# Optimization experiments

Hardware: AMD Instinct MI355X
Metric: run time of the kernel (lower is better)

Reference implementation:

```python
import jax, jax.numpy as jnp
import numpy as np

B, S, N, F = 4, 8, 1024, 6
H, L, K, D = 64, 3, 16, 3  # hidden, layers, neighbors, num_dims
EPS = 1e-6


def setup_inputs() -> dict:
    key = jax.random.key(0)
    ks = iter(jax.random.split(key, 64))

    def w(shape, fan_in):
        return jax.random.normal(next(ks), shape, jnp.float32) / np.sqrt(fan_in)

    inp = {
        'points': jax.random.normal(next(ks), (B, S, N, F), jnp.float32),
        'w_in': w((F, H), F), 'b_in': jnp.zeros((H,), jnp.float32),
        # stacked per-layer params for the 3 PointTransformerLayers
        'Wq': w((L, H, H), H), 'bq': jnp.zeros((L, H), jnp.float32),
        'Wk': w((L, H, H), H), 'bk': jnp.zeros((L, H), jnp.float32),
        'Wv': w((L, H, H), H), 'bv': jnp.zeros((L, H), jnp.float32),
        'Wpe': w((L, D, H), D), 'bpe': jnp.zeros((L, H), jnp.float32),
        'Wpd': w((L, D, H), D), 'bpd': jnp.zeros((L, H), jnp.float32),
        'Wa': w((L, H, 1), H), 'ba': jnp.zeros((L, 1), jnp.float32),
        'Wo': w((L, H, H), H), 'bo': jnp.zeros((L, H), jnp.float32),
        'ln_s': jnp.ones((L, H), jnp.float32), 'ln_b': jnp.zeros((L, H), jnp.float32),
        # EncoderTransformerLayer params
        'Wek': w((H, H), H), 'bek': jnp.zeros((H,), jnp.float32),
        'Weq': w((H, H), H), 'beq': jnp.zeros((H,), jnp.float32),
        'Wev': w((H, H), H), 'bev': jnp.zeros((H,), jnp.float32),
        'We1': w((H, H), H), 'be1': jnp.zeros((H,), jnp.float32),
        'We2': w((H, H), H), 'be2': jnp.zeros((H,), jnp.float32),
        'ln2_s': jnp.ones((H,), jnp.float32), 'ln2_b': jnp.zeros((H,), jnp.float32),
    }
    return inp


def _layernorm(x, scale, bias):
    mu = jnp.mean(x, axis=-1, keepdims=True)
    var = jnp.var(x, axis=-1, keepdims=True)
    return (x - mu) * jax.lax.rsqrt(var + EPS) * scale + bias


def _point_layer(x, pos, Wq, bq, Wk, bk, Wv, bv, Wpe, bpe, Wpd, bpd, Wa, ba, Wo, bo):
    # x: [B,S,N,H], pos: [B,S,N,3]
    q = x @ Wq + bq
    k = x @ Wk + bk
    v = x @ Wv + bv
    pos_enc = pos @ Wpe + bpe  # [B,S,N,H]
    # pairwise squared distances: diff[i,j] = pos[i] - pos[j]
    pos_diff = pos[..., :, None, :] - pos[..., None, :, :]  # [B,S,N,N,3]
    dist = jnp.sum(pos_diff ** 2, axis=-1)                  # [B,S,N,N]
    _, nidx = jax.lax.top_k(-dist, K)                       # [B,S,N,K]

    def gather(a):  # a: [B,S,N,C] -> [B,S,N,K,C]
        return jnp.take_along_axis(a[:, :, None], nidx[..., None], axis=3)

    k_n = gather(k)
    v_n = gather(v)
    p_n = gather(pos_enc)
    qp = (q + pos_enc)[..., None, :]                        # [B,S,N,1,H]
    pd_enc = (gather(pos) - pos[..., None, :]) @ Wpd + bpd  # [B,S,N,K,H]
    scale = jnp.sqrt(jnp.float32(H))
    attn = qp * (k_n + p_n + pd_enc) / scale                # [B,S,N,K,H]
    attn = (attn @ Wa + ba).squeeze(-1)                     # [B,S,N,K]
    attn = jax.nn.softmax(attn, axis=-1)
    out = jnp.sum(attn[..., None] * v_n, axis=-2)           # [B,S,N,H]
    out = jax.nn.gelu(out @ Wo + bo)
    return x + out


def _encoder_layer(x, Wek, bek, Weq, beq, Wev, bev, We1, be1, We2, be2):
    k = x @ Wek + bek
    q = x @ Weq + beq
    v = x @ Wev + bev
    aw = jnp.einsum('bth,bsh->bts', q, k)
    aw = jax.nn.softmax(aw / jnp.sqrt(jnp.float32(H)), axis=-1)
    out = jnp.einsum('bts,bsh->bth', aw, v)
    out = jax.nn.gelu(out @ We1 + be1) @ We2 + be2
    return x + out


def reference(points, w_in, b_in, Wq, bq, Wk, bk, Wv, bv, Wpe, bpe, Wpd, bpd,
              Wa, ba, Wo, bo, ln_s, ln_b, Wek, bek, Weq, beq, Wev, bev,
              We1, be1, We2, be2, ln2_s, ln2_b):
    pos = points[..., :D]
    x = points @ w_in + b_in
    for i in range(L):
        x = _point_layer(x, pos, Wq[i], bq[i], Wk[i], bk[i], Wv[i], bv[i],
                         Wpe[i], bpe[i], Wpd[i], bpd[i], Wa[i], ba[i], Wo[i], bo[i])
        x = _layernorm(x, ln_s[i], ln_b[i])
    x = jnp.max(x, axis=-2)  # pool over points -> [B,S,H]
    x = _encoder_layer(x, Wek, bek, Weq, beq, Wev, bev, We1, be1, We2, be2)
    x = _layernorm(x, ln2_s, ln2_b)
    x = jnp.max(x, axis=-2)  # pool over seq -> [B,H]
    return x
```

## Files before the change

kernel.cpp:

```cpp
#include <hip/hip_runtime.h>
#include <cfloat>
#include <cmath>
#include <cstdint>

#define NPT   1024
#define NCL   32
#define PTOT  32768
#define HH    64
#define KNN_K 16
#define KNN_BLKS (NCL * 256)

#define RFL(x) __builtin_amdgcn_readfirstlane(x)

__device__ __forceinline__ float wave_sum64(float t) {
#pragma unroll
  for (int o = 32; o > 0; o >>= 1) t += __shfl_xor(t, o, 64);
  return t;
}

template <int NV>
__device__ __forceinline__ float mreduce(const float (&P)[NV], int lane) {
  float buf[NV];
#pragma unroll
  for (int i = 0; i < NV; ++i) buf[i] = P[i];
#pragma unroll
  for (int s = 0; (1 << s) < NV; ++s) {
    bool hi = (lane & (1 << s)) != 0;
#pragma unroll
    for (int m = 0; m < (NV >> (s + 1)); ++m) {
      float a = buf[2 * m], b = buf[2 * m + 1];
      float keep = hi ? b : a;
      float send = hi ? a : b;
      buf[m] = keep + __shfl_xor(send, 1 << s, 64);
    }
  }
  float t = buf[0];
#pragma unroll
  for (int o = NV; o < 64; o <<= 1) t += __shfl_xor(t, o, 64);
  return t;
}

__device__ __forceinline__ float gelu_f(float z) {
  float zc = 0.7978845608028654f * (z + 0.044715f * z * z * z);
  float t = __expf(2.0f * zc);
  float th = 1.0f - 2.0f / (t + 1.0f);
  return 0.5f * z * (1.0f + th);
}

__global__ __launch_bounds__(256) void k_front(
    const float* __restrict__ pts, const float* __restrict__ w_in,
    const float* __restrict__ b_in, float* __restrict__ x,
    float* __restrict__ pos4, int* __restrict__ nidx) {
  if (blockIdx.x >= KNN_BLKS) {
    int b2 = blockIdx.x - KNN_BLKS;
    int vb = (b2 & 7) * 1024 + (b2 >> 3);
    int p = vb * 4 + (threadIdx.x >> 6);
    int h = threadIdx.x & 63;
    const float* pp = pts + p * 6;
    float acc = b_in[h];
#pragma unroll
    for (int f = 0; f < 6; ++f) acc += pp[f] * w_in[f * HH + h];
    x[p * HH + h] = acc;
    if (h < 4) pos4[p * 4 + h] = (h < 3) ? pp[h] : 0.0f;
    return;
  }

  __shared__ float4 sp[NPT];
  int cloud = blockIdx.x >> 8;
  int qbase = (blockIdx.x & 255) * 4;
  const float* cp = pts + (size_t)cloud * NPT * 6;
  for (int j = threadIdx.x; j < NPT; j += 256) {
    const float* q = cp + j * 6;
    sp[j] = make_float4(q[0], q[1], q[2], 0.0f);
  }
  __syncthreads();

  int wv = threadIdx.x >> 6;
  int lane = threadIdx.x & 63;
  int i = qbase + wv;
  float4 qp = sp[i];

  unsigned du[16];
#pragma unroll
  for (int c = 0; c < 16; ++c) {
    float4 pj = sp[c * 64 + lane];
    float dx = qp.x - pj.x, dy = qp.y - pj.y, dz = qp.z - pj.z;
    float d2 = __fadd_rn(__fadd_rn(__fmul_rn(dx, dx), __fmul_rn(dy, dy)),
                         __fmul_rn(dz, dz));
    du[c] = __float_as_uint(d2);
  }

  unsigned t = 0u;
#pragma unroll
  for (int bit = 30; bit >= 15; --bit) {
    unsigned tp = t | (1u << bit);
    int cnt = 0;
#pragma unroll
    for (int c = 0; c < 16; ++c)
      cnt += __popcll(__ballot(du[c] < tp));
    if (cnt <= 15) t = tp;
  }

  int obase = (cloud * NPT + i) * KNN_K;
  unsigned long long below = (1ull << lane) - 1ull;
  int slot = 0;
#pragma unroll
  for (int c = 0; c < 16; ++c) {
    bool lt = du[c] < t;
    unsigned long long m = __ballot(lt);
    if (lt) {
      int off = __popcll(m & below);
      nidx[obase + slot + off] = c * 64 + lane;
    }
    slot += __popcll(m);
  }

  int erem = KNN_K - slot;
  unsigned hi_end = t + (1u << 15);
  unsigned bu[16];
#pragma unroll
  for (int c = 0; c < 16; ++c)
    bu[c] = (du[c] >= t && du[c] < hi_end) ? du[c] : 0xFFFFFFFFu;
  for (int r2 = 0; r2 < erem; ++r2) {
    unsigned bd = bu[0];
    int bc = 0;
#pragma unroll
    for (int c = 1; c < 16; ++c) {
      if (bu[c] < bd) { bd = bu[c]; bc = c; }
    }
    unsigned gd = bd;
#pragma unroll
    for (int o = 32; o > 0; o >>= 1) {
      unsigned g2 = (unsigned)__shfl_xor((int)gd, o, 64);
      gd = (g2 < gd) ? g2 : gd;
    }
    int myidx = bc * 64 + lane;
    int gidx = (bd == gd) ? myidx : 0x7fffffff;
#pragma unroll
    for (int o = 32; o > 0; o >>= 1) {
      int g2 = __shfl_xor(gidx, o, 64);
      gidx = (g2 < gidx) ? g2 : gidx;
    }
    if (lane == 0) nidx[obase + slot + r2] = gidx;
    int sel = (myidx == gidx) ? bc : 99;
#pragma unroll
    for (int c = 0; c < 16; ++c) bu[c] = (c == sel) ? 0xFFFFFFFFu : bu[c];
  }
}

__global__ __launch_bounds__(256) void k_qkv_gemm(
    const float* __restrict__ x, const float* __restrict__ pos4,
    const float* __restrict__ Wq, const float* __restrict__ bq,
    const float* __restrict__ Wk, const float* __restrict__ bk,
    const float* __restrict__ Wv, const float* __restrict__ bv,
    const float* __restrict__ Wpe, const float* __restrict__ bpe,
    const float* __restrict__ Wpd, const float* __restrict__ bpd,
    float* __restrict__ qq, float* __restrict__ kkv) {
  __shared__ float w_lds[3][HH][HH];
  int lane = threadIdx.x & 63;
  int wv = threadIdx.x >> 6;
  int bid = blockIdx.x;
  int vb = (bid & 7) * 128 + (bid >> 3);
  int pb = RFL(vb * 32 + wv * 8);
  const float* xw = x + (size_t)pb * HH;
  const float4* posw = reinterpret_cast<const float4*>(pos4) + pb;

  {
    float4* dst = reinterpret_cast<float4*>(&w_lds[0][0][0]);
    const float4* s0 = reinterpret_cast<const float4*>(Wq);
    const float4* s1 = reinterpret_cast<const float4*>(Wk);
    const float4* s2 = reinterpret_cast<const float4*>(Wv);
#pragma unroll
    for (int i = 0; i < 4; ++i) {
      int idx = i * 256 + threadIdx.x;
      dst[idx] = s0[idx];
      dst[1024 + idx] = s1[idx];
      dst[2048 + idx] = s2[idx];
    }
  }
  __syncthreads();

  float wpe0 = Wpe[lane], wpe1 = Wpe[HH + lane], wpe2 = Wpe[2 * HH + lane];
  float wpd0 = Wpd[lane], wpd1 = Wpd[HH + lane], wpd2 = Wpd[2 * HH + lane];
  float we0 = wpe0 + wpd0, we1 = wpe1 + wpd1, we2 = wpe2 + wpd2;
  float bqq = bq[lane] + bpe[lane];
  float bkk = bk[lane] + bpe[lane] + bpd[lane];
  float bvv = bv[lane];

  float aq[8], ak[8], av[8];
#pragma unroll
  for (int p = 0; p < 8; ++p) { aq[p] = bqq; ak[p] = bkk; av[p] = bvv; }

#pragma unroll
  for (int c = 0; c < 8; ++c) {
    float wq8[8], wk8[8], wv8[8];
#pragma unroll
    for (int j = 0; j < 8; ++j) {
      int g = c * 8 + j;
      wq8[j] = w_lds[0][g][lane];
      wk8[j] = w_lds[1][g][lane];
      wv8[j] = w_lds[2][g][lane];
    }
#pragma unroll
    for (int p = 0; p < 8; ++p) {
#pragma unroll
      for (int j = 0; j < 8; ++j) {
        float xv = xw[p * HH + c * 8 + j];
        aq[p] = fmaf(xv, wq8[j], aq[p]);
        ak[p] = fmaf(xv, wk8[j], ak[p]);
        av[p] = fmaf(xv, wv8[j], av[p]);
      }
    }
  }

#pragma unroll
  for (int p = 0; p < 8; ++p) {
    float4 pp = posw[p];
    float qv = aq[p] + pp.x * wpe0 + pp.y * wpe1 + pp.z * wpe2;
    float kv = ak[p] + pp.x * we0 + pp.y * we1 + pp.z * we2;
    qq[(size_t)(pb + p) * HH + lane] = qv;
    reinterpret_cast<float2*>(kkv + ((size_t)(pb + p) << 7))[lane] =
        make_float2(kv, av[p]);
  }
}

__global__ __launch_bounds__(256) void k_attn_core(
    float* __restrict__ qq, const float* __restrict__ kkv,
    const int* __restrict__ nidx, const float* __restrict__ pos4,
    const float* __restrict__ Wpd, const float* __restrict__ Wa,
    const float* __restrict__ ba) {
  int lane = threadIdx.x & 63;
  int bid = blockIdx.x;
  int vb = (bid & 7) * 1024 + (bid >> 3);
  int pu = RFL(vb * 4 + (threadIdx.x >> 6));
  int cbase = pu & ~(NPT - 1);

  float4 pp = reinterpret_cast<const float4*>(pos4)[pu];
  float u = qq[(size_t)pu * HH + lane] * Wa[lane] * 0.125f;
  float pdq = pp.x * Wpd[lane] + pp.y * Wpd[HH + lane] + pp.z * Wpd[2 * HH + lane];
  float C0 = wave_sum64(u * pdq) - ba[0];

  const int4* niw = reinterpret_cast<const int4*>(nidx + (size_t)pu * KNN_K);
  int nj[KNN_K];
#pragma unroll
  for (int g = 0; g < 4; ++g) {
    int4 r = niw[g];
    nj[g * 4 + 0] = r.x; nj[g * 4 + 1] = r.y;
    nj[g * 4 + 2] = r.z; nj[g * 4 + 3] = r.w;
  }

  float vj[KNN_K], P[KNN_K];
#pragma unroll
  for (int jj = 0; jj < KNN_K; ++jj) {
    float2 kv = reinterpret_cast<const float2*>(
        kkv + ((size_t)(cbase + nj[jj]) << 7))[lane];
    vj[jj] = kv.y;
    P[jj] = u * kv.x;
  }

  float T = mreduce<16>(P, lane);
  float lg = T - C0;

  float mx = lg;
#pragma unroll
  for (int o = 1; o < 16; o <<= 1) mx = fmaxf(mx, __shfl_xor(mx, o, 64));
  float e = __expf(lg - mx);
  float s = e;
#pragma unroll
  for (int o = 1; o < 16; o <<= 1) s += __shfl_xor(s, o, 64);

  float oacc = 0.f;
  int sb = lane & 48;
#pragma unroll
  for (int jj = 0; jj < KNN_K; ++jj)
    oacc = fmaf(__shfl(e, sb | jj, 64), vj[jj], oacc);

  qq[(size_t)pu * HH + lane] = oacc / s;
}

__global__ __launch_bounds__(256) void k_wo_ln(
    const float* __restrict__ outb, const float* __restrict__ Wo,
    const float* __restrict__ bo, float* __restrict__ x,
    const float* __restrict__ ln_s, const float* __restrict__ ln_b,
    float* __restrict__ partial, int do_pool) {
  __shared__ float w_lds[HH][HH];
  __shared__ float red[4][HH];
  int lane = threadIdx.x & 63;
  int wv = threadIdx.x >> 6;
  int bid = blockIdx.x;
  int vb = (bid & 7) * 128 + (bid >> 3);
  int pb = RFL(vb * 32 + wv * 8);
  const float* ow = outb + (size_t)pb * HH;

  {
    float4* dst = reinterpret_cast<float4*>(&w_lds[0][0]);
    const float4* src = reinterpret_cast<const float4*>(Wo);
#pragma unroll
    for (int i = 0; i < 4; ++i) {
      int idx = i * 256 + threadIdx.x;
      dst[idx] = src[idx];
    }
  }
  __syncthreads();

  float acc[8];
  float b0 = bo[lane];
#pragma unroll
  for (int p = 0; p < 8; ++p) acc[p] = b0;

#pragma unroll
  for (int c = 0; c < 8; ++c) {
    float w8[8];
#pragma unroll
    for (int j = 0; j < 8; ++j) w8[j] = w_lds[c * 8 + j][lane];
#pragma unroll
    for (int p = 0; p < 8; ++p) {
#pragma unroll
      for (int j = 0; j < 8; ++j) {
        float ov = ow[p * HH + c * 8 + j];
        acc[p] = fmaf(ov, w8[j], acc[p]);
      }
    }
  }

  float sg = ln_s[lane], bg = ln_b[lane];
  float xn[8];
#pragma unroll
  for (int p = 0; p < 8; ++p)
    xn[p] = x[(size_t)(pb + p) * HH + lane] + gelu_f(acc[p]);

  float Ts = mreduce<8>(xn, lane);
  float dd[8], sq[8];
#pragma unroll
  for (int p = 0; p < 8; ++p) {
    float mu = __shfl(Ts, p, 64) * (1.0f / HH);
    dd[p] = xn[p] - mu;
    sq[p] = dd[p] * dd[p];
  }
  float Tv = mreduce<8>(sq, lane);
  float mxp = -FLT_MAX;
#pragma unroll
  for (int p = 0; p < 8; ++p) {
    float var = __shfl(Tv, p, 64) * (1.0f / HH);
    float yv = dd[p] * rsqrtf(var + 1e-6f) * sg + bg;
    x[(size_t)(pb + p) * HH + lane] = yv;
    mxp = fmaxf(mxp, yv);
  }

  if (do_pool) {
    red[wv][lane] = mxp;
    __syncthreads();
    if (wv == 0) {
      float m = fmaxf(fmaxf(red[0][lane], red[1][lane]),
                      fmaxf(red[2][lane], red[3][lane]));
      partial[(size_t)vb * HH + lane] = m;
    }
  }
}

__global__ __launch_bounds__(512) void k_enc(
    const float* __restrict__ partial,
    const float* __restrict__ Wek, const float* __restrict__ bek,
    const float* __restrict__ Weq, const float* __restrict__ beq,
    const float* __restrict__ Wev, const float* __restrict__ bev,
    const float* __restrict__ We1, const float* __restrict__ be1,
    const float* __restrict__ We2, const float* __restrict__ be2,
    const float* __restrict__ ln2_s, const float* __restrict__ ln2_b,
    float* __restrict__ out) {
  __shared__ float xs[8][HH], ks[8][HH], vs[8][HH], x2[8][HH];
  int b = blockIdx.x;
  int t = threadIdx.x >> 6;
  int h = threadIdx.x & 63;
  {
    int ci = b * 8 + t;
    const float* pp = partial + (size_t)ci * 32 * HH + h;
    float mx = pp[0];
#pragma unroll
    for (int c8 = 1; c8 < 32; ++c8) mx = fmaxf(mx, pp[c8 * HH]);
    xs[t][h] = mx;
  }
  __syncthreads();

  float kk = bek[h], qq = beq[h], vv = bev[h];
#pragma unroll 8
  for (int g = 0; g < HH; ++g) {
    float xv = xs[t][g];
    kk += xv * Wek[g * HH + h];
    qq += xv * Weq[g * HH + h];
    vv += xv * Wev[g * HH + h];
  }
  ks[t][h] = kk;
  vs[t][h] = vv;
  __syncthreads();

  float logit[8];
#pragma unroll
  for (int s = 0; s < 8; ++s) {
    float tt = qq * ks[s][h];
    logit[s] = wave_sum64(tt) * 0.125f;
  }
  float m = logit[0];
#pragma unroll
  for (int s = 1; s < 8; ++s) m = fmaxf(m, logit[s]);
  float ssum = 0.f;
#pragma unroll
  for (int s = 0; s < 8; ++s) { logit[s] = expf(logit[s] - m); ssum += logit[s]; }
  float o = 0.f;
#pragma unroll
  for (int s = 0; s < 8; ++s) o += (logit[s] / ssum) * vs[s][h];

  float h1 = be1[h];
#pragma unroll 8
  for (int g = 0; g < HH; ++g) h1 += __shfl(o, g, 64) * We1[g * HH + h];
  h1 = gelu_f(h1);
  float h2 = be2[h];
#pragma unroll 8
  for (int g = 0; g < HH; ++g) h2 += __shfl(h1, g, 64) * We2[g * HH + h];

  float xn = xs[t][h] + h2;
  float mu = wave_sum64(xn) * (1.0f / HH);
  float d = xn - mu;
  float var = wave_sum64(d * d) * (1.0f / HH);
  float yv = d * rsqrtf(var + 1e-6f) * ln2_s[h] + ln2_b[h];
  x2[t][h] = yv;
  __syncthreads();
  if (t == 0) {
    float mm = x2[0][h];
#pragma unroll
    for (int s = 1; s < 8; ++s) mm = fmaxf(mm, x2[s][h]);
    out[b * HH + h] = mm;
  }
}

extern "C" void kernel_launch(void* const* d_in, const int* in_sizes, int n_in,
                              void* d_out, int out_size, void* d_ws, size_t ws_size,
                              hipStream_t stream) {
  const float* points = (const float*)d_in[0];
  const float* w_in   = (const float*)d_in[1];
  const float* b_in   = (const float*)d_in[2];
  const float* Wq     = (const float*)d_in[3];
  const float* bq     = (const float*)d_in[4];
  const float* Wk     = (const float*)d_in[5];
  const float* bk     = (const float*)d_in[6];
  const float* Wv     = (const float*)d_in[7];
  const float* bv     = (const float*)d_in[8];
  const float* Wpe    = (const float*)d_in[9];
  const float* bpe    = (const float*)d_in[10];
  const float* Wpd    = (const float*)d_in[11];
  const float* bpd    = (const float*)d_in[12];
  const float* Wa     = (const float*)d_in[13];
  const float* ba     = (const float*)d_in[14];
  const float* Wo     = (const float*)d_in[15];
  const float* bo     = (const float*)d_in[16];
  const float* ln_s   = (const float*)d_in[17];
  const float* ln_b   = (const float*)d_in[18];
  const float* Wek    = (const float*)d_in[19];
  const float* bek    = (const float*)d_in[20];
  const float* Weq    = (const float*)d_in[21];
  const float* beq    = (const float*)d_in[22];
  const float* Wev    = (const float*)d_in[23];
  const float* bev    = (const float*)d_in[24];
  const float* We1    = (const float*)d_in[25];
  const float* be1    = (const float*)d_in[26];
  const float* We2    = (const float*)d_in[27];
  const float* be2    = (const float*)d_in[28];
  const float* ln2_s  = (const float*)d_in[29];
  const float* ln2_b  = (const float*)d_in[30];

  float* ws      = (float*)d_ws;
  float* pos4    = ws;
  float* xbuf    = pos4 + 4 * PTOT;
  float* qbuf    = xbuf + 64 * PTOT;
  float* kkv     = qbuf + 64 * PTOT;
  float* partial = kkv + 128 * PTOT;
  int*   nidx    = (int*)(partial + 2048 * HH);

  k_front<<<KNN_BLKS + PTOT / 4, 256, 0, stream>>>(points, w_in, b_in,
                                                   xbuf, pos4, nidx);

  for (int l = 0; l < 3; ++l) {
    k_qkv_gemm<<<1024, 256, 0, stream>>>(xbuf, pos4,
        Wq + l * HH * HH, bq + l * HH,
        Wk + l * HH * HH, bk + l * HH,
        Wv + l * HH * HH, bv + l * HH,
        Wpe + l * 3 * HH, bpe + l * HH,
        Wpd + l * 3 * HH, bpd + l * HH,
        qbuf, kkv);
    k_attn_core<<<PTOT / 4, 256, 0, stream>>>(qbuf, kkv, nidx, pos4,
        Wpd + l * 3 * HH, Wa + l * HH, ba + l);
    k_wo_ln<<<1024, 256, 0, stream>>>(qbuf,
        Wo + l * HH * HH, bo + l * HH, xbuf,
        ln_s + l * HH, ln_b + l * HH, partial, l == 2 ? 1 : 0);
  }

  k_enc<<<4, 512, 0, stream>>>(partial, Wek, bek, Weq, beq, Wev, bev,
                               We1, be1, We2, be2, ln2_s, ln2_b, (float*)d_out);
}
```

Before: 218.8 us.

## Fuse attention with Wo/LayerNorm and input projection with first QKV GEMM

Splits kNN into its own kernel, with each block handling 32 queries (8 per wave) so the shared-memory point load is amortised. The input projection is fused into the layer-0 QKV GEMM. The attention core is fused with the Wo projection, GELU and LayerNorm in one wave-per-point kernel, which removes the round trip of the attention output through global memory and one launch per layer. The cost is that Wo is now read directly from global/cache per wave rather than staged in LDS. Pooling partials grow 4x, so the encoder's reduction loop lengthens from 32 to 256 steps.

```diff
diff --git a/kernel.cpp b/kernel.cpp
--- a/kernel.cpp
+++ b/kernel.cpp
@@ -8,7 +8,6 @@
 #define PTOT  32768
 #define HH    64
 #define KNN_K 16
-#define KNN_BLKS (NCL * 256)
 
 #define RFL(x) __builtin_amdgcn_readfirstlane(x)
 
@@ -47,27 +46,11 @@
   return 0.5f * z * (1.0f + th);
 }
 
-__global__ __launch_bounds__(256) void k_front(
-    const float* __restrict__ pts, const float* __restrict__ w_in,
-    const float* __restrict__ b_in, float* __restrict__ x,
-    float* __restrict__ pos4, int* __restrict__ nidx) {
-  if (blockIdx.x >= KNN_BLKS) {
-    int b2 = blockIdx.x - KNN_BLKS;
-    int vb = (b2 & 7) * 1024 + (b2 >> 3);
-    int p = vb * 4 + (threadIdx.x >> 6);
-    int h = threadIdx.x & 63;
-    const float* pp = pts + p * 6;
-    float acc = b_in[h];
-#pragma unroll
-    for (int f = 0; f < 6; ++f) acc += pp[f] * w_in[f * HH + h];
-    x[p * HH + h] = acc;
-    if (h < 4) pos4[p * 4 + h] = (h < 3) ? pp[h] : 0.0f;
-    return;
-  }
-
+__global__ __launch_bounds__(256) void k_knn(const float* __restrict__ pts,
+                                             int* __restrict__ nidx) {
   __shared__ float4 sp[NPT];
-  int cloud = blockIdx.x >> 8;
-  int qbase = (blockIdx.x & 255) * 4;
+  int cloud = blockIdx.x >> 5;
+  int qbase = (blockIdx.x & 31) * 32;
   const float* cp = pts + (size_t)cloud * NPT * 6;
   for (int j = threadIdx.x; j < NPT; j += 256) {
     const float* q = cp + j * 6;
@@ -77,74 +60,167 @@
 
   int wv = threadIdx.x >> 6;
   int lane = threadIdx.x & 63;
-  int i = qbase + wv;
-  float4 qp = sp[i];
-
-  unsigned du[16];
-#pragma unroll
-  for (int c = 0; c < 16; ++c) {
-    float4 pj = sp[c * 64 + lane];
-    float dx = qp.x - pj.x, dy = qp.y - pj.y, dz = qp.z - pj.z;
-    float d2 = __fadd_rn(__fadd_rn(__fmul_rn(dx, dx), __fmul_rn(dy, dy)),
-                         __fmul_rn(dz, dz));
-    du[c] = __float_as_uint(d2);
-  }
-
-  unsigned t = 0u;
-#pragma unroll
-  for (int bit = 30; bit >= 15; --bit) {
-    unsigned tp = t | (1u << bit);
-    int cnt = 0;
+
+  for (int qi = 0; qi < 8; ++qi) {
+    int i = qbase + wv * 8 + qi;
+    float4 qp = sp[i];
+
+    unsigned du[16];
+#pragma unroll
+    for (int c = 0; c < 16; ++c) {
+      float4 pj = sp[c * 64 + lane];
+      float dx = qp.x - pj.x, dy = qp.y - pj.y, dz = qp.z - pj.z;
+      float d2 = __fadd_rn(__fadd_rn(__fmul_rn(dx, dx), __fmul_rn(dy, dy)),
+                           __fmul_rn(dz, dz));
+      du[c] = __float_as_uint(d2);
+    }
+
+    unsigned t = 0u;
+#pragma unroll
+    for (int bit = 30; bit >= 15; --bit) {
+      unsigned tp = t | (1u << bit);
+      int cnt = 0;
+#pragma unroll
+      for (int c = 0; c < 16; ++c)
+        cnt += __popcll(__ballot(du[c] < tp));
+      if (cnt <= 15) t = tp;
+    }
+
+    int obase = (cloud * NPT + i) * KNN_K;
+    unsigned long long below = (1ull << lane) - 1ull;
+    int slot = 0;
+#pragma unroll
+    for (int c = 0; c < 16; ++c) {
+      bool lt = du[c] < t;
+      unsigned long long m = __ballot(lt);
+      if (lt) nidx[obase + slot + __popcll(m & below)] = c * 64 + lane;
+      slot += __popcll(m);
+    }
+
+    int erem = KNN_K - slot;
+    unsigned hi_end = t + (1u << 15);
+    unsigned bu[16];
 #pragma unroll
     for (int c = 0; c < 16; ++c)
-      cnt += __popcll(__ballot(du[c] < tp));
-    if (cnt <= 15) t = tp;
-  }
-
-  int obase = (cloud * NPT + i) * KNN_K;
-  unsigned long long below = (1ull << lane) - 1ull;
-  int slot = 0;
-#pragma unroll
-  for (int c = 0; c < 16; ++c) {
-    bool lt = du[c] < t;
-    unsigned long long m = __ballot(lt);
-    if (lt) {
-      int off = __popcll(m & below);
-      nidx[obase + slot + off] = c * 64 + lane;
-    }
-    slot += __popcll(m);
-  }
-
-  int erem = KNN_K - slot;
-  unsigned hi_end = t + (1u << 15);
-  unsigned bu[16];
-#pragma unroll
-  for (int c = 0; c < 16; ++c)
-    bu[c] = (du[c] >= t && du[c] < hi_end) ? du[c] : 0xFFFFFFFFu;
-  for (int r2 = 0; r2 < erem; ++r2) {
-    unsigned bd = bu[0];
-    int bc = 0;
-#pragma unroll
-    for (int c = 1; c < 16; ++c) {
-      if (bu[c] < bd) { bd = bu[c]; bc = c; }
-    }
-    unsigned gd = bd;
-#pragma unroll
-    for (int o = 32; o > 0; o >>= 1) {
-      unsigned g2 = (unsigned)__shfl_xor((int)gd, o, 64);
-      gd = (g2 < gd) ? g2 : gd;
-    }
-    int myidx = bc * 64 + lane;
-    int gidx = (bd == gd) ? myidx : 0x7fffffff;
-#pragma unroll
-    for (int o = 32; o > 0; o >>= 1) {
-      int g2 = __shfl_xor(gidx, o, 64);
-      gidx = (g2 < gidx) ? g2 : gidx;
-    }
-    if (lane == 0) nidx[obase + slot + r2] = gidx;
-    int sel = (myidx == gidx) ? bc : 99;
-#pragma unroll
-    for (int c = 0; c < 16; ++c) bu[c] = (c == sel) ? 0xFFFFFFFFu : bu[c];
+      bu[c] = (du[c] >= t && du[c] < hi_end) ? du[c] : 0xFFFFFFFFu;
+    for (int r2 = 0; r2 < erem; ++r2) {
+      unsigned bd = bu[0];
+      int bc = 0;
+#pragma unroll
+      for (int c = 1; c < 16; ++c)
+        if (bu[c] < bd) { bd = bu[c]; bc = c; }
+      unsigned gd = bd;
+#pragma unroll
+      for (int o = 32; o > 0; o >>= 1) {
+        unsigned g2 = (unsigned)__shfl_xor((int)gd, o, 64);
+        gd = (g2 < gd) ? g2 : gd;
+      }
+      int myidx = bc * 64 + lane;
+      int gidx = (bd == gd) ? myidx : 0x7fffffff;
+#pragma unroll
+      for (int o = 32; o > 0; o >>= 1) {
+        int g2 = __shfl_xor(gidx, o, 64);
+        gidx = (g2 < gidx) ? g2 : gidx;
+      }
+      if (lane == 0) nidx[obase + slot + r2] = gidx;
+      int sel = (myidx == gidx) ? bc : 99;
+#pragma unroll
+      for (int c = 0; c < 16; ++c) bu[c] = (c == sel) ? 0xFFFFFFFFu : bu[c];
+    }
+  }
+}
+
+__global__ __launch_bounds__(256) void k_qkv0(
+    const float* __restrict__ pts,
+    const float* __restrict__ w_in, const float* __restrict__ b_in,
+    const float* __restrict__ Wq, const float* __restrict__ bq,
+    const float* __restrict__ Wk, const float* __restrict__ bk,
+    const float* __restrict__ Wv, const float* __restrict__ bv,
+    const float* __restrict__ Wpe, const float* __restrict__ bpe,
+    const float* __restrict__ Wpd, const float* __restrict__ bpd,
+    float* __restrict__ x, float* __restrict__ pos4,
+    float* __restrict__ qq, float* __restrict__ kkv) {
+  __shared__ float w_lds[3][HH][HH];
+  int lane = threadIdx.x & 63;
+  int wv = threadIdx.x >> 6;
+  int bid = blockIdx.x;
+  int vb = (bid & 7) * 128 + (bid >> 3);
+  int pb = RFL(vb * 32 + wv * 8);
+
+  {
+    float4* dst = reinterpret_cast<float4*>(&w_lds[0][0][0]);
+    const float4* s0 = reinterpret_cast<const float4*>(Wq);
+    const float4* s1 = reinterpret_cast<const float4*>(Wk);
+    const float4* s2 = reinterpret_cast<const float4*>(Wv);
+#pragma unroll
+    for (int i = 0; i < 4; ++i) {
+      int idx = i * 256 + threadIdx.x;
+      dst[idx] = s0[idx];
+      dst[1024 + idx] = s1[idx];
+      dst[2048 + idx] = s2[idx];
+    }
+  }
+
+  float xr[8];
+  float bi = b_in[lane];
+  float w0 = w_in[lane], w1 = w_in[HH + lane], w2 = w_in[2 * HH + lane];
+  float w3 = w_in[3 * HH + lane], w4 = w_in[4 * HH + lane], w5 = w_in[5 * HH + lane];
+  float px[8], py[8], pz[8];
+#pragma unroll
+  for (int p = 0; p < 8; ++p) {
+    int gp = pb + p;
+    const float* pp = pts + (size_t)gp * 6;
+    float f0 = pp[0], f1 = pp[1], f2 = pp[2], f3 = pp[3], f4 = pp[4], f5 = pp[5];
+    float acc = bi;
+    acc += f0 * w0; acc += f1 * w1; acc += f2 * w2;
+    acc += f3 * w3; acc += f4 * w4; acc += f5 * w5;
+    xr[p] = acc;
+    x[(size_t)gp * HH + lane] = acc;
+    px[p] = f0; py[p] = f1; pz[p] = f2;
+    if (lane < 4) pos4[(size_t)gp * 4 + lane] = (lane < 3) ? pp[lane] : 0.0f;
+  }
+  __syncthreads();
+
+  float wpe0 = Wpe[lane], wpe1 = Wpe[HH + lane], wpe2 = Wpe[2 * HH + lane];
+  float wpd0 = Wpd[lane], wpd1 = Wpd[HH + lane], wpd2 = Wpd[2 * HH + lane];
+  float we0 = wpe0 + wpd0, we1 = wpe1 + wpd1, we2 = wpe2 + wpd2;
+  float bqq = bq[lane] + bpe[lane];
+  float bkk = bk[lane] + bpe[lane] + bpd[lane];
+  float bvv = bv[lane];
+
+  float aq[8], ak[8], av[8];
+#pragma unroll
+  for (int p = 0; p < 8; ++p) { aq[p] = bqq; ak[p] = bkk; av[p] = bvv; }
+
+#pragma unroll
+  for (int c = 0; c < 8; ++c) {
+    float wq8[8], wk8[8], wv8[8];
+#pragma unroll
+    for (int j = 0; j < 8; ++j) {
+      int g = c * 8 + j;
+      wq8[j] = w_lds[0][g][lane];
+      wk8[j] = w_lds[1][g][lane];
+      wv8[j] = w_lds[2][g][lane];
+    }
+#pragma unroll
+    for (int p = 0; p < 8; ++p) {
+#pragma unroll
+      for (int j = 0; j < 8; ++j) {
+        float xv = __shfl(xr[p], c * 8 + j, 64);
+        aq[p] = fmaf(xv, wq8[j], aq[p]);
+        ak[p] = fmaf(xv, wk8[j], ak[p]);
+        av[p] = fmaf(xv, wv8[j], av[p]);
+      }
+    }
+  }
+
+#pragma unroll
+  for (int p = 0; p < 8; ++p) {
+    float qv = aq[p] + px[p] * wpe0 + py[p] * wpe1 + pz[p] * wpe2;
+    float kv = ak[p] + px[p] * we0 + py[p] * we1 + pz[p] * we2;
+    qq[(size_t)(pb + p) * HH + lane] = qv;
+    reinterpret_cast<float2*>(kkv + ((size_t)(pb + p) << 7))[lane] =
+        make_float2(kv, av[p]);
   }
 }
 
@@ -224,15 +300,20 @@
   }
 }
 
-__global__ __launch_bounds__(256) void k_attn_core(
-    float* __restrict__ qq, const float* __restrict__ kkv,
+__global__ __launch_bounds__(256) void k_awl(
+    const float* __restrict__ qq, const float* __restrict__ kkv,
     const int* __restrict__ nidx, const float* __restrict__ pos4,
     const float* __restrict__ Wpd, const float* __restrict__ Wa,
-    const float* __restrict__ ba) {
+    const float* __restrict__ ba,
+    const float* __restrict__ Wo, const float* __restrict__ bo,
+    const float* __restrict__ ln_s, const float* __restrict__ ln_b,
+    float* __restrict__ x, float* __restrict__ partial, int do_pool) {
+  __shared__ float red[4][HH];
   int lane = threadIdx.x & 63;
+  int wv = threadIdx.x >> 6;
   int bid = blockIdx.x;
   int vb = (bid & 7) * 1024 + (bid >> 3);
-  int pu = RFL(vb * 4 + (threadIdx.x >> 6));
+  int pu = RFL(vb * 4 + wv);
   int cbase = pu & ~(NPT - 1);
 
   float4 pp = reinterpret_cast<const float4*>(pos4)[pu];
@@ -260,7 +341,6 @@
 
   float T = mreduce<16>(P, lane);
   float lg = T - C0;
-
   float mx = lg;
 #pragma unroll
   for (int o = 1; o < 16; o <<= 1) mx = fmaxf(mx, __shfl_xor(mx, o, 64));
@@ -268,87 +348,35 @@
   float s = e;
 #pragma unroll
   for (int o = 1; o < 16; o <<= 1) s += __shfl_xor(s, o, 64);
-
   float oacc = 0.f;
   int sb = lane & 48;
 #pragma unroll
   for (int jj = 0; jj < KNN_K; ++jj)
     oacc = fmaf(__shfl(e, sb | jj, 64), vj[jj], oacc);
-
-  qq[(size_t)pu * HH + lane] = oacc / s;
-}
-
-__global__ __launch_bounds__(256) void k_wo_ln(
-    const float* __restrict__ outb, const float* __restrict__ Wo,
-    const float* __restrict__ bo, float* __restrict__ x,
-    const float* __restrict__ ln_s, const float* __restrict__ ln_b,
-    float* __restrict__ partial, int do_pool) {
-  __shared__ float w_lds[HH][HH];
-  __shared__ float red[4][HH];
-  int lane = threadIdx.x & 63;
-  int wv = threadIdx.x >> 6;
-  int bid = blockIdx.x;
-  int vb = (bid & 7) * 128 + (bid >> 3);
-  int pb = RFL(vb * 32 + wv * 8);
-  const float* ow = outb + (size_t)pb * HH;
-
-  {
-    float4* dst = reinterpret_cast<float4*>(&w_lds[0][0]);
-    const float4* src = reinterpret_cast<const float4*>(Wo);
-#pragma unroll
-    for (int i = 0; i < 4; ++i) {
-      int idx = i * 256 + threadIdx.x;
-      dst[idx] = src[idx];
-    }
-  }
-  __syncthreads();
-
-  float acc[8];
-  float b0 = bo[lane];
-#pragma unroll
-  for (int p = 0; p < 8; ++p) acc[p] = b0;
-
+  float out = oacc / s;
+
+  float acc = bo[lane];
 #pragma unroll
   for (int c = 0; c < 8; ++c) {
     float w8[8];
 #pragma unroll
-    for (int j = 0; j < 8; ++j) w8[j] = w_lds[c * 8 + j][lane];
-#pragma unroll
-    for (int p = 0; p < 8; ++p) {
-#pragma unroll
-      for (int j = 0; j < 8; ++j) {
-        float ov = ow[p * HH + c * 8 + j];
-        acc[p] = fmaf(ov, w8[j], acc[p]);
-      }
-    }
-  }
-
-  float sg = ln_s[lane], bg = ln_b[lane];
-  float xn[8];
-#pragma unroll
-  for (int p = 0; p < 8; ++p)
-    xn[p] = x[(size_t)(pb + p) * HH + lane] + gelu_f(acc[p]);
-
-  float Ts = mreduce<8>(xn, lane);
-  float dd[8], sq[8];
-#pragma unroll
-  for (int p = 0; p < 8; ++p) {
-    float mu = __shfl(Ts, p, 64) * (1.0f / HH);
-    dd[p] = xn[p] - mu;
-    sq[p] = dd[p] * dd[p];
-  }
-  float Tv = mreduce<8>(sq, lane);
-  float mxp = -FLT_MAX;
-#pragma unroll
-  for (int p = 0; p < 8; ++p) {
-    float var = __shfl(Tv, p, 64) * (1.0f / HH);
-    float yv = dd[p] * rsqrtf(var + 1e-6f) * sg + bg;
-    x[(size_t)(pb + p) * HH + lane] = yv;
-    mxp = fmaxf(mxp, yv);
-  }
+    for (int j = 0; j < 8; ++j) w8[j] = Wo[(c * 8 + j) * HH + lane];
+#pragma unroll
+    for (int j = 0; j < 8; ++j) {
+      float og = __shfl(out, c * 8 + j, 64);
+      acc = fmaf(og, w8[j], acc);
+    }
+  }
+
+  float xn = x[(size_t)pu * HH + lane] + gelu_f(acc);
+  float mu = wave_sum64(xn) * (1.0f / HH);
+  float dd = xn - mu;
+  float var = wave_sum64(dd * dd) * (1.0f / HH);
+  float yv = dd * rsqrtf(var + 1e-6f) * ln_s[lane] + ln_b[lane];
+  x[(size_t)pu * HH + lane] = yv;
 
   if (do_pool) {
-    red[wv][lane] = mxp;
+    red[wv][lane] = yv;
     __syncthreads();
     if (wv == 0) {
       float m = fmaxf(fmaxf(red[0][lane], red[1][lane]),
@@ -373,10 +401,10 @@
   int h = threadIdx.x & 63;
   {
     int ci = b * 8 + t;
-    const float* pp = partial + (size_t)ci * 32 * HH + h;
+    const float* pp = partial + (size_t)ci * 256 * HH + h;
     float mx = pp[0];
-#pragma unroll
-    for (int c8 = 1; c8 < 32; ++c8) mx = fmaxf(mx, pp[c8 * HH]);
+#pragma unroll 8
+    for (int c8 = 1; c8 < 256; ++c8) mx = fmaxf(mx, pp[c8 * HH]);
     xs[t][h] = mx;
   }
   __syncthreads();
@@ -473,24 +501,23 @@
   float* qbuf    = xbuf + 64 * PTOT;
   float* kkv     = qbuf + 64 * PTOT;
   float* partial = kkv + 128 * PTOT;
-  int*   nidx    = (int*)(partial + 2048 * HH);
-
-  k_front<<<KNN_BLKS + PTOT / 4, 256, 0, stream>>>(points, w_in, b_in,
-                                                   xbuf, pos4, nidx);
+  int*   nidx    = (int*)(partial + 8192 * HH);
+
+  k_knn<<<NCL * 32, 256, 0, stream>>>(points, nidx);
+
+  k_qkv0<<<1024, 256, 0, stream>>>(points, w_in, b_in,
+      Wq, bq, Wk, bk, Wv, bv, Wpe, bpe, Wpd, bpd,
+      xbuf, pos4, qbuf, kkv);
 
   for (int l = 0; l < 3; ++l) {
-    k_qkv_gemm<<<1024, 256, 0, stream>>>(xbuf, pos4,
-        Wq + l * HH * HH, bq + l * HH,
-        Wk + l * HH * HH, bk + l * HH,
-        Wv + l * HH * HH, bv + l * HH,
-        Wpe + l * 3 * HH, bpe + l * HH,
-        Wpd + l * 3 * HH, bpd + l * HH,
-        qbuf, kkv);
-    k_attn_core<<<PTOT / 4, 256, 0, stream>>>(qbuf, kkv, nidx, pos4,
-        Wpd + l * 3 * HH, Wa + l * HH, ba + l);
-    k_wo_ln<<<1024, 256, 0, stream>>>(qbuf,
-        Wo + l * HH * HH, bo + l * HH, xbuf,
-        ln_s + l * HH, ln_b + l * HH, partial, l == 2 ? 1 : 0);
+    if (l > 0)
+      k_qkv_gemm<<<1024, 256, 0, stream>>>(xbuf, pos4,
+          Wq + l * 4096, bq + l * 64, Wk + l * 4096, bk + l * 64,
+          Wv + l * 4096, bv + l * 64, Wpe + l * 192, bpe + l * 64,
+          Wpd + l * 192, bpd + l * 64, qbuf, kkv);
+    k_awl<<<8192, 256, 0, stream>>>(qbuf, kkv, nidx, pos4,
+        Wpd + l * 192, Wa + l * 64, ba + l, Wo + l * 4096, bo + l * 64,
+        ln_s + l * 64, ln_b + l * 64, xbuf, partial, l == 2 ? 1 : 0);
   }
 
   k_enc<<<4, 512, 0, stream>>>(partial, Wek, bek, Weq, beq, Wev, bev,
```

Result: slower. 323.8 us (+48.0%).

## Fuse next layer's QKV projection into the Wo+LayerNorm kernel

Applied to the files above, without the earlier changes.

The Wo projection + LayerNorm kernel now also computes the next layer's Q, K and V projections from the normalized rows still held in registers. This removes two separate QKV GEMM launches and the re-read of x between them. Wo is now read directly from global memory instead of LDS, and the LDS holds the three QKV weight matrices. LDS use grows to 48KB per block, which may lower occupancy, and the in-register projection relies on many shuffles.

```diff
diff --git a/kernel.cpp b/kernel.cpp
--- a/kernel.cpp
+++ b/kernel.cpp
@@ -108,10 +108,7 @@
   for (int c = 0; c < 16; ++c) {
     bool lt = du[c] < t;
     unsigned long long m = __ballot(lt);
-    if (lt) {
-      int off = __popcll(m & below);
-      nidx[obase + slot + off] = c * 64 + lane;
-    }
+    if (lt) nidx[obase + slot + __popcll(m & below)] = c * 64 + lane;
     slot += __popcll(m);
   }
 
@@ -125,9 +122,8 @@
     unsigned bd = bu[0];
     int bc = 0;
 #pragma unroll
-    for (int c = 1; c < 16; ++c) {
+    for (int c = 1; c < 16; ++c)
       if (bu[c] < bd) { bd = bu[c]; bc = c; }
-    }
     unsigned gd = bd;
 #pragma unroll
     for (int o = 32; o > 0; o >>= 1) {
@@ -278,30 +274,40 @@
   qq[(size_t)pu * HH + lane] = oacc / s;
 }
 
-__global__ __launch_bounds__(256) void k_wo_ln(
-    const float* __restrict__ outb, const float* __restrict__ Wo,
-    const float* __restrict__ bo, float* __restrict__ x,
+__global__ __launch_bounds__(256) void k_wol_qkv(
+    float* __restrict__ qq, const float* __restrict__ pos4,
+    const float* __restrict__ Wo, const float* __restrict__ bo,
     const float* __restrict__ ln_s, const float* __restrict__ ln_b,
-    float* __restrict__ partial, int do_pool) {
-  __shared__ float w_lds[HH][HH];
+    float* __restrict__ x,
+    const float* __restrict__ Wq, const float* __restrict__ bq,
+    const float* __restrict__ Wk, const float* __restrict__ bk,
+    const float* __restrict__ Wv, const float* __restrict__ bv,
+    const float* __restrict__ Wpe, const float* __restrict__ bpe,
+    const float* __restrict__ Wpd, const float* __restrict__ bpd,
+    float* __restrict__ kkv, float* __restrict__ partial,
+    int do_qkv, int do_pool) {
+  __shared__ float w_lds[3][HH][HH];
   __shared__ float red[4][HH];
   int lane = threadIdx.x & 63;
   int wv = threadIdx.x >> 6;
   int bid = blockIdx.x;
   int vb = (bid & 7) * 128 + (bid >> 3);
   int pb = RFL(vb * 32 + wv * 8);
-  const float* ow = outb + (size_t)pb * HH;
-
-  {
-    float4* dst = reinterpret_cast<float4*>(&w_lds[0][0]);
-    const float4* src = reinterpret_cast<const float4*>(Wo);
+  const float* ow = qq + (size_t)pb * HH;
+
+  if (do_qkv) {
+    float4* dst = reinterpret_cast<float4*>(&w_lds[0][0][0]);
+    const float4* s0 = reinterpret_cast<const float4*>(Wq);
+    const float4* s1 = reinterpret_cast<const float4*>(Wk);
+    const float4* s2 = reinterpret_cast<const float4*>(Wv);
 #pragma unroll
     for (int i = 0; i < 4; ++i) {
       int idx = i * 256 + threadIdx.x;
-      dst[idx] = src[idx];
-    }
-  }
-  __syncthreads();
+      dst[idx] = s0[idx];
+      dst[1024 + idx] = s1[idx];
+      dst[2048 + idx] = s2[idx];
+    }
+  }
 
   float acc[8];
   float b0 = bo[lane];
@@ -312,7 +318,7 @@
   for (int c = 0; c < 8; ++c) {
     float w8[8];
 #pragma unroll
-    for (int j = 0; j < 8; ++j) w8[j] = w_lds[c * 8 + j][lane];
+    for (int j = 0; j < 8; ++j) w8[j] = Wo[(c * 8 + j) * HH + lane];
 #pragma unroll
     for (int p = 0; p < 8; ++p) {
 #pragma unroll
@@ -338,13 +344,60 @@
     sq[p] = dd[p] * dd[p];
   }
   float Tv = mreduce<8>(sq, lane);
+  float yv[8];
   float mxp = -FLT_MAX;
 #pragma unroll
   for (int p = 0; p < 8; ++p) {
     float var = __shfl(Tv, p, 64) * (1.0f / HH);
-    float yv = dd[p] * rsqrtf(var + 1e-6f) * sg + bg;
-    x[(size_t)(pb + p) * HH + lane] = yv;
-    mxp = fmaxf(mxp, yv);
+    yv[p] = dd[p] * rsqrtf(var + 1e-6f) * sg + bg;
+    x[(size_t)(pb + p) * HH + lane] = yv[p];
+    mxp = fmaxf(mxp, yv[p]);
+  }
+
+  if (do_qkv) {
+    __syncthreads();
+    float wpe0 = Wpe[lane], wpe1 = Wpe[HH + lane], wpe2 = Wpe[2 * HH + lane];
+    float wpd0 = Wpd[lane], wpd1 = Wpd[HH + lane], wpd2 = Wpd[2 * HH + lane];
+    float we0 = wpe0 + wpd0, we1 = wpe1 + wpd1, we2 = wpe2 + wpd2;
+    float bqq = bq[lane] + bpe[lane];
+    float bkk = bk[lane] + bpe[lane] + bpd[lane];
+    float bvv = bv[lane];
+
+    float aq[8], ak[8], av[8];
+#pragma unroll
+    for (int p = 0; p < 8; ++p) { aq[p] = bqq; ak[p] = bkk; av[p] = bvv; }
+
+#pragma unroll
+    for (int c = 0; c < 8; ++c) {
+      float wq8[8], wk8[8], wv8[8];
+#pragma unroll
+      for (int j = 0; j < 8; ++j) {
+        int g = c * 8 + j;
+        wq8[j] = w_lds[0][g][lane];
+        wk8[j] = w_lds[1][g][lane];
+        wv8[j] = w_lds[2][g][lane];
+      }
+#pragma unroll
+      for (int p = 0; p < 8; ++p) {
+#pragma unroll
+        for (int j = 0; j < 8; ++j) {
+          float xv = __shfl(yv[p], c * 8 + j, 64);
+          aq[p] = fmaf(xv, wq8[j], aq[p]);
+          ak[p] = fmaf(xv, wk8[j], ak[p]);
+          av[p] = fmaf(xv, wv8[j], av[p]);
+        }
+      }
+    }
+
+#pragma unroll
+    for (int p = 0; p < 8; ++p) {
+      float4 pp = reinterpret_cast<const float4*>(pos4)[pb + p];
+      float qv = aq[p] + pp.x * wpe0 + pp.y * wpe1 + pp.z * wpe2;
+      float kv = ak[p] + pp.x * we0 + pp.y * we1 + pp.z * we2;
+      qq[(size_t)(pb + p) * HH + lane] = qv;
+      reinterpret_cast<float2*>(kkv + ((size_t)(pb + p) << 7))[lane] =
+          make_float2(kv, av[p]);
+    }
   }
 
   if (do_pool) {
@@ -478,19 +531,19 @@
   k_front<<<KNN_BLKS + PTOT / 4, 256, 0, stream>>>(points, w_in, b_in,
                                                    xbuf, pos4, nidx);
 
+  k_qkv_gemm<<<1024, 256, 0, stream>>>(xbuf, pos4,
+      Wq, bq, Wk, bk, Wv, bv, Wpe, bpe, Wpd, bpd, qbuf, kkv);
+
   for (int l = 0; l < 3; ++l) {
-    k_qkv_gemm<<<1024, 256, 0, stream>>>(xbuf, pos4,
-        Wq + l * HH * HH, bq + l * HH,
-        Wk + l * HH * HH, bk + l * HH,
-        Wv + l * HH * HH, bv + l * HH,
-        Wpe + l * 3 * HH, bpe + l * HH,
-        Wpd + l * 3 * HH, bpd + l * HH,
-        qbuf, kkv);
-    k_attn_core<<<PTOT / 4, 256, 0, stream>>>(qbuf, kkv, nidx, pos4,
-        Wpd + l * 3 * HH, Wa + l * HH, ba + l);
-    k_wo_ln<<<1024, 256, 0, stream>>>(qbuf,
-        Wo + l * HH * HH, bo + l * HH, xbuf,
-        ln_s + l * HH, ln_b + l * HH, partial, l == 2 ? 1 : 0);
+    k_attn_core<<<8192, 256, 0, stream>>>(qbuf, kkv, nidx, pos4,
+        Wpd + l * 192, Wa + l * 64, ba + l);
+    int nl = (l < 2) ? (l + 1) : 0;
+    k_wol_qkv<<<1024, 256, 0, stream>>>(qbuf, pos4,
+        Wo + l * 4096, bo + l * 64, ln_s + l * 64, ln_b + l * 64, xbuf,
+        Wq + nl * 4096, bq + nl * 64, Wk + nl * 4096, bk + nl * 64,
+        Wv + nl * 4096, bv + nl * 64, Wpe + nl * 192, bpe + nl * 64,
+        Wpd + nl * 192, bpd + nl * 64,
+        kkv, partial, l < 2 ? 1 : 0, l == 2 ? 1 : 0);
   }
 
   k_enc<<<4, 512, 0, stream>>>(partial, Wek, bek, Weq, beq, Wev, bev,
```

After: 241.9 us. 1.11x slower.
